# Kernel tuning notes

Hardware: AMD Instinct MI355X
Metric: run time of the kernel (lower is better)

The kernel has to match this reference:

```python
import jax, jax.numpy as jnp
import numpy as np

B, N, G, T = 512, 10000, 2048, 131072  # batch, gene sets, agg groups, total flat indices

def setup_inputs() -> dict:
    key = jax.random.key(0)
    k1, k2, k3 = jax.random.split(key, 3)
    gene_set_features = jax.random.normal(k1, (B, N), dtype=jnp.float32)
    flat_indices = jax.random.randint(k2, (T,), 0, N)          # which gene-set column each slot reads
    segment_ids = jnp.sort(jax.random.randint(k3, (T,), 0, G))  # which agg group each slot belongs to
    return {"gene_set_features": gene_set_features,
            "flat_indices": flat_indices,
            "segment_ids": segment_ids,
            "num_groups": G}

def reference(gene_set_features, flat_indices, segment_ids, num_groups):
    # Ragged per-group mean pooling (pooling_type='mean'), CSR-style in one pass.
    gathered = gene_set_features[:, flat_indices]            # [B, T]
    sums = jax.ops.segment_sum(gathered.T, segment_ids,
                               num_segments=num_groups)      # [G, B]
    counts = jax.ops.segment_sum(jnp.ones((flat_indices.shape[0],),
                                          dtype=gene_set_features.dtype),
                                 segment_ids, num_segments=num_groups)  # [G]
    means = sums / jnp.maximum(counts, 1.0)[:, None]         # empty groups -> 0, matching zeros init
    return means.T                                           # [B, G]
```

## Files before the change

### kernel.cpp

```cpp
#include <hip/hip_runtime.h>


__device__ __forceinline__ unsigned bf16rne(float f) {
    unsigned u = __float_as_uint(f);
    return (u + 0x7fffu + ((u >> 16) & 1u)) >> 16;
}

__global__ __launch_bounds__(256) void pa_prep(const float* __restrict__ feat,
                                               const int* __restrict__ seg,
                                               unsigned short* __restrict__ featT,
                                               int* __restrict__ offs,
                                               int N, int T, int G, int nXBlocks) {
    if (blockIdx.y == 8) {
        int stride = nXBlocks * 256;
        for (int t = blockIdx.x * 256 + threadIdx.x; t < T; t += stride) {
            int cur  = seg[t];
            int prev = (t == 0) ? -1 : seg[t - 1];
            for (int g = prev + 1; g <= cur; ++g) offs[g] = t;
            if (t == T - 1) {
                for (int g = cur + 1; g <= G; ++g) offs[g] = T;
            }
        }
        return;
    }

    __shared__ float tile[64][65];
    const int n0 = blockIdx.x * 64;
    const int b0 = blockIdx.y * 64;
    const int tid = threadIdx.x;
    const int r  = tid >> 4;
    const int c4 = tid & 15;

    if (n0 + 64 <= N) {
        #pragma unroll
        for (int i = 0; i < 4; ++i) {
            int b = r + 16 * i;
            const float4 v = *(const float4*)&feat[(size_t)(b0 + b) * N + n0 + c4 * 4];
            tile[b][c4 * 4 + 0] = v.x;
            tile[b][c4 * 4 + 1] = v.y;
            tile[b][c4 * 4 + 2] = v.z;
            tile[b][c4 * 4 + 3] = v.w;
        }
    } else {
        #pragma unroll
        for (int i = 0; i < 4; ++i) {
            int b = r + 16 * i;
            #pragma unroll
            for (int j = 0; j < 4; ++j) {
                int n = n0 + c4 * 4 + j;
                tile[b][c4 * 4 + j] = (n < N) ? feat[(size_t)(b0 + b) * N + n] : 0.0f;
            }
        }
    }
    __syncthreads();

    uint2* outu = (uint2*)featT;
    #pragma unroll
    for (int i = 0; i < 4; ++i) {
        int nl = r + 16 * i;
        int n = n0 + nl;
        if (n >= N) continue;
        uint2 u;
        u.x = bf16rne(tile[c4 * 4 + 0][nl]) | (bf16rne(tile[c4 * 4 + 1][nl]) << 16);
        u.y = bf16rne(tile[c4 * 4 + 2][nl]) | (bf16rne(tile[c4 * 4 + 3][nl]) << 16);
        outu[(size_t)n * 128 + (b0 >> 2) + c4] = u;
    }
}

#define ACC8(v)                                   \
    do {                                          \
        a0 += __uint_as_float((v).x << 16);       \
        a1 += __uint_as_float((v).x);             \
        a2 += __uint_as_float((v).y << 16);       \
        a3 += __uint_as_float((v).y);             \
        a4 += __uint_as_float((v).z << 16);       \
        a5 += __uint_as_float((v).z);             \
        a6 += __uint_as_float((v).w << 16);       \
        a7 += __uint_as_float((v).w);             \
    } while (0)

__global__ __launch_bounds__(256) void pa_gather_mean_bf16(
    const unsigned short* __restrict__ featT,
    const int* __restrict__ idxs,
    const int* __restrict__ offs,
    float* __restrict__ out,
    int G) {
    const int chunk = blockIdx.x & 7;
    const int wave  = threadIdx.x >> 6;
    const int g     = (blockIdx.x >> 3) * 4 + wave;
    const int lane  = threadIdx.x & 63;
    const int lane_b = lane & 7;
    const int slot   = lane >> 3;

    const int s = offs[g];
    const int e = offs[g + 1];
    const int cnt = e - s;

    const char* __restrict__ fbase = (const char*)featT + chunk * 128 + lane_b * 16;

    float a0 = 0.f, a1 = 0.f, a2 = 0.f, a3 = 0.f,
          a4 = 0.f, a5 = 0.f, a6 = 0.f, a7 = 0.f;

    int w = s;
    int nrem = cnt;
    int myidx = (s + lane < e) ? idxs[s + lane] : 0;

    while (nrem >= 64) {
        int cur = myidx;
        w += 64;
        nrem -= 64;
        if (nrem > 0) myidx = (w + lane < e) ? idxs[w + lane] : 0;
        #pragma unroll
        for (int k = 0; k < 8; ++k) {
            int ridx = __shfl(cur, slot + 8 * k);
            uint4 v = *(const uint4*)(fbase + ((size_t)(unsigned)(ridx << 10)));
            ACC8(v);
        }
    }
    if (nrem > 0) {
        int cur = myidx;
        #pragma unroll
        for (int k = 0; k < 8; ++k) {
            int li = slot + 8 * k;
            int ridx = __shfl(cur, li);
            if (li < nrem) {
                uint4 v = *(const uint4*)(fbase + ((size_t)(unsigned)(ridx << 10)));
                ACC8(v);
            }
        }
    }

    a0 += __shfl_xor(a0, 8); a0 += __shfl_xor(a0, 16); a0 += __shfl_xor(a0, 32);
    a1 += __shfl_xor(a1, 8); a1 += __shfl_xor(a1, 16); a1 += __shfl_xor(a1, 32);
    a2 += __shfl_xor(a2, 8); a2 += __shfl_xor(a2, 16); a2 += __shfl_xor(a2, 32);
    a3 += __shfl_xor(a3, 8); a3 += __shfl_xor(a3, 16); a3 += __shfl_xor(a3, 32);
    a4 += __shfl_xor(a4, 8); a4 += __shfl_xor(a4, 16); a4 += __shfl_xor(a4, 32);
    a5 += __shfl_xor(a5, 8); a5 += __shfl_xor(a5, 16); a5 += __shfl_xor(a5, 32);
    a6 += __shfl_xor(a6, 8); a6 += __shfl_xor(a6, 16); a6 += __shfl_xor(a6, 32);
    a7 += __shfl_xor(a7, 8); a7 += __shfl_xor(a7, 16); a7 += __shfl_xor(a7, 32);

    __shared__ float tile[4][64];
    if (slot == 0) {
        float inv = 1.0f / (float)(cnt > 0 ? cnt : 1);
        int bl = lane_b * 8;
        tile[wave][bl + 0] = a0 * inv;
        tile[wave][bl + 1] = a1 * inv;
        tile[wave][bl + 2] = a2 * inv;
        tile[wave][bl + 3] = a3 * inv;
        tile[wave][bl + 4] = a4 * inv;
        tile[wave][bl + 5] = a5 * inv;
        tile[wave][bl + 6] = a6 * inv;
        tile[wave][bl + 7] = a7 * inv;
    }
    __syncthreads();

    int b_local = threadIdx.x >> 2;
    int gi      = threadIdx.x & 3;
    int gg      = (blockIdx.x >> 3) * 4 + gi;
    out[(size_t)(chunk * 64 + b_local) * G + gg] = tile[gi][b_local];
}

__global__ __launch_bounds__(256) void pa_group_mean_direct(
    const float* __restrict__ feat, const int* __restrict__ flat_indices,
    const int* __restrict__ segment_ids, float* __restrict__ out,
    int T, int B, int N, int G) {
    const int g = blockIdx.x;
    const int tid = threadIdx.x;
    __shared__ int sb[2];
    __shared__ int s_idx[256];
    if (tid < 2) {
        int target = g + tid;
        int lo = 0, hi = T;
        while (lo < hi) {
            int mid = (lo + hi) >> 1;
            if (segment_ids[mid] < target) lo = mid + 1; else hi = mid;
        }
        sb[tid] = lo;
    }
    __syncthreads();
    const int s = sb[0], e = sb[1];
    const int cnt = e - s;
    int b0 = tid * 2, b1 = tid * 2 + 1;
    float x0 = 0.f, x1 = 0.f;
    for (int base = s; base < e; base += 256) {
        int k = base + tid;
        if (k < e) s_idx[tid] = flat_indices[k];
        __syncthreads();
        int m = min(256, e - base);
        for (int jj = 0; jj < m; ++jj) {
            int idx = s_idx[jj];
            if (b0 < B) x0 += feat[(long)b0 * N + idx];
            if (b1 < B) x1 += feat[(long)b1 * N + idx];
        }
        __syncthreads();
    }
    float inv = 1.0f / (float)(cnt > 0 ? cnt : 1);
    if (b0 < B) out[(long)b0 * G + g] = x0 * inv;
    if (b1 < B) out[(long)b1 * G + g] = x1 * inv;
}

extern "C" void kernel_launch(void* const* d_in, const int* in_sizes, int n_in,
                              void* d_out, int out_size, void* d_ws, size_t ws_size,
                              hipStream_t stream) {
    const float* feat          = (const float*)d_in[0];
    const int*   flat_indices  = (const int*)d_in[1];
    const int*   segment_ids   = (const int*)d_in[2];
    float*       out           = (float*)d_out;

    const int B = 512;
    const int N = in_sizes[0] / B;
    const int T = in_sizes[1];
    const int G = out_size / B;

    size_t featT_bytes = (size_t)N * B * sizeof(unsigned short);
    size_t need = featT_bytes + (size_t)(G + 1) * sizeof(int);
    if (ws_size >= need && B == 512 && (G % 4) == 0 && T >= 1) {
        unsigned short* featT = (unsigned short*)d_ws;
        int* offs = (int*)((char*)d_ws + featT_bytes);

        int nXBlocks = (N + 63) / 64;
        dim3 g1(nXBlocks, 9);
        pa_prep<<<g1, 256, 0, stream>>>(feat, segment_ids, featT, offs, N, T, G, nXBlocks);

        pa_gather_mean_bf16<<<(G / 4) * 8, 256, 0, stream>>>(featT, flat_indices, offs,
                                                             out, G);
    } else {
        pa_group_mean_direct<<<G, 256, 0, stream>>>(feat, flat_indices, segment_ids,
                                                    out, T, B, N, G);
    }
}
```

Measured before the change: 26.51 us.

## Process two groups per wave in gather and flatten prep grid ordering

The gather kernel now gives each wave two segment groups with separate accumulator sets, interleaving their 64-index windows so more independent loads are in flight. It launches half as many blocks and writes output as float2. The prep kernel switches to a 1D grid where the 8 batch chunks for one N tile are adjacent, and the offset-building blocks sit at the end. This trades more registers and some load imbalance between paired groups for more memory-level parallelism per wave.

```diff
diff --git a/kernel.cpp b/kernel.cpp
--- a/kernel.cpp
+++ b/kernel.cpp
@@ -10,10 +10,13 @@
                                                const int* __restrict__ seg,
                                                unsigned short* __restrict__ featT,
                                                int* __restrict__ offs,
-                                               int N, int T, int G, int nXBlocks) {
-    if (blockIdx.y == 8) {
-        int stride = nXBlocks * 256;
-        for (int t = blockIdx.x * 256 + threadIdx.x; t < T; t += stride) {
+                                               int N, int T, int G, int nTiles) {
+    const int x = blockIdx.x;
+    const int nTr = nTiles * 8;
+    if (x >= nTr) {
+        int s = x - nTr;
+        if (s >= 157) return;
+        for (int t = s * 256 + threadIdx.x; t < T; t += 157 * 256) {
             int cur  = seg[t];
             int prev = (t == 0) ? -1 : seg[t - 1];
             for (int g = prev + 1; g <= cur; ++g) offs[g] = t;
@@ -25,8 +28,9 @@
     }
 
     __shared__ float tile[64][65];
-    const int n0 = blockIdx.x * 64;
-    const int b0 = blockIdx.y * 64;
+    const int c  = x & 7;
+    const int n0 = (x >> 3) * 64;
+    const int b0 = c * 64;
     const int tid = threadIdx.x;
     const int r  = tid >> 4;
     const int c4 = tid & 15;
@@ -67,7 +71,7 @@
     }
 }
 
-#define ACC8(v)                                   \
+#define ACC8(v, a0, a1, a2, a3, a4, a5, a6, a7)   \
     do {                                          \
         a0 += __uint_as_float((v).x << 16);       \
         a1 += __uint_as_float((v).x);             \
@@ -79,6 +83,32 @@
         a7 += __uint_as_float((v).w);             \
     } while (0)
 
+#define FULLWIN(cur, a0, a1, a2, a3, a4, a5, a6, a7)                         \
+    do {                                                                     \
+        _Pragma("unroll")                                                    \
+        for (int k = 0; k < 8; ++k) {                                        \
+            int ridx = __shfl((cur), slot + 8 * k);                          \
+            uint4 v = *(const uint4*)(fbase + ((size_t)(unsigned)(ridx << 10))); \
+            ACC8(v, a0, a1, a2, a3, a4, a5, a6, a7);                         \
+        }                                                                    \
+    } while (0)
+
+#define TAILWIN(cur, nr, a0, a1, a2, a3, a4, a5, a6, a7)                     \
+    do {                                                                     \
+        _Pragma("unroll")                                                    \
+        for (int k = 0; k < 8; ++k) {                                        \
+            int li = slot + 8 * k;                                           \
+            int ridx = __shfl((cur), li);                                    \
+            if (li < (nr)) {                                                 \
+                uint4 v = *(const uint4*)(fbase + ((size_t)(unsigned)(ridx << 10))); \
+                ACC8(v, a0, a1, a2, a3, a4, a5, a6, a7);                     \
+            }                                                                \
+        }                                                                    \
+    } while (0)
+
+#define RED8(a) \
+    a += __shfl_xor(a, 8); a += __shfl_xor(a, 16); a += __shfl_xor(a, 32)
+
 __global__ __launch_bounds__(256) void pa_gather_mean_bf16(
     const unsigned short* __restrict__ featT,
     const int* __restrict__ idxs,
@@ -86,78 +116,88 @@
     float* __restrict__ out,
     int G) {
     const int chunk = blockIdx.x & 7;
+    const int i     = blockIdx.x >> 3;
     const int wave  = threadIdx.x >> 6;
-    const int g     = (blockIdx.x >> 3) * 4 + wave;
     const int lane  = threadIdx.x & 63;
     const int lane_b = lane & 7;
     const int slot   = lane >> 3;
 
-    const int s = offs[g];
-    const int e = offs[g + 1];
-    const int cnt = e - s;
+    const int g0 = i * 8 + wave * 2;
+    const int g1 = g0 + 1;
+    const int s0 = offs[g0], e0 = offs[g0 + 1];
+    const int s1 = offs[g1], e1 = offs[g1 + 1];
+    const int cnt0 = e0 - s0, cnt1 = e1 - s1;
 
     const char* __restrict__ fbase = (const char*)featT + chunk * 128 + lane_b * 16;
 
     float a0 = 0.f, a1 = 0.f, a2 = 0.f, a3 = 0.f,
           a4 = 0.f, a5 = 0.f, a6 = 0.f, a7 = 0.f;
-
-    int w = s;
-    int nrem = cnt;
-    int myidx = (s + lane < e) ? idxs[s + lane] : 0;
-
-    while (nrem >= 64) {
-        int cur = myidx;
-        w += 64;
-        nrem -= 64;
-        if (nrem > 0) myidx = (w + lane < e) ? idxs[w + lane] : 0;
-        #pragma unroll
-        for (int k = 0; k < 8; ++k) {
-            int ridx = __shfl(cur, slot + 8 * k);
-            uint4 v = *(const uint4*)(fbase + ((size_t)(unsigned)(ridx << 10)));
-            ACC8(v);
-        }
-    }
-    if (nrem > 0) {
-        int cur = myidx;
-        #pragma unroll
-        for (int k = 0; k < 8; ++k) {
-            int li = slot + 8 * k;
-            int ridx = __shfl(cur, li);
-            if (li < nrem) {
-                uint4 v = *(const uint4*)(fbase + ((size_t)(unsigned)(ridx << 10)));
-                ACC8(v);
-            }
-        }
-    }
-
-    a0 += __shfl_xor(a0, 8); a0 += __shfl_xor(a0, 16); a0 += __shfl_xor(a0, 32);
-    a1 += __shfl_xor(a1, 8); a1 += __shfl_xor(a1, 16); a1 += __shfl_xor(a1, 32);
-    a2 += __shfl_xor(a2, 8); a2 += __shfl_xor(a2, 16); a2 += __shfl_xor(a2, 32);
-    a3 += __shfl_xor(a3, 8); a3 += __shfl_xor(a3, 16); a3 += __shfl_xor(a3, 32);
-    a4 += __shfl_xor(a4, 8); a4 += __shfl_xor(a4, 16); a4 += __shfl_xor(a4, 32);
-    a5 += __shfl_xor(a5, 8); a5 += __shfl_xor(a5, 16); a5 += __shfl_xor(a5, 32);
-    a6 += __shfl_xor(a6, 8); a6 += __shfl_xor(a6, 16); a6 += __shfl_xor(a6, 32);
-    a7 += __shfl_xor(a7, 8); a7 += __shfl_xor(a7, 16); a7 += __shfl_xor(a7, 32);
-
-    __shared__ float tile[4][64];
+    float b0 = 0.f, b1 = 0.f, b2 = 0.f, b3 = 0.f,
+          b4 = 0.f, b5 = 0.f, b6 = 0.f, b7 = 0.f;
+
+    int w0 = s0, n0 = cnt0;
+    int w1 = s1, n1 = cnt1;
+    int id0 = (w0 + lane < e0) ? idxs[w0 + lane] : 0;
+    int id1 = (w1 + lane < e1) ? idxs[w1 + lane] : 0;
+
+    while (n0 >= 64 && n1 >= 64) {
+        int c0 = id0, c1 = id1;
+        w0 += 64; n0 -= 64;
+        w1 += 64; n1 -= 64;
+        if (n0 > 0) id0 = (w0 + lane < e0) ? idxs[w0 + lane] : 0;
+        if (n1 > 0) id1 = (w1 + lane < e1) ? idxs[w1 + lane] : 0;
+        FULLWIN(c0, a0, a1, a2, a3, a4, a5, a6, a7);
+        FULLWIN(c1, b0, b1, b2, b3, b4, b5, b6, b7);
+    }
+    while (n0 >= 64) {
+        int c0 = id0;
+        w0 += 64; n0 -= 64;
+        if (n0 > 0) id0 = (w0 + lane < e0) ? idxs[w0 + lane] : 0;
+        FULLWIN(c0, a0, a1, a2, a3, a4, a5, a6, a7);
+    }
+    while (n1 >= 64) {
+        int c1 = id1;
+        w1 += 64; n1 -= 64;
+        if (n1 > 0) id1 = (w1 + lane < e1) ? idxs[w1 + lane] : 0;
+        FULLWIN(c1, b0, b1, b2, b3, b4, b5, b6, b7);
+    }
+    if (n0 > 0) TAILWIN(id0, n0, a0, a1, a2, a3, a4, a5, a6, a7);
+    if (n1 > 0) TAILWIN(id1, n1, b0, b1, b2, b3, b4, b5, b6, b7);
+
+    RED8(a0); RED8(a1); RED8(a2); RED8(a3); RED8(a4); RED8(a5); RED8(a6); RED8(a7);
+    RED8(b0); RED8(b1); RED8(b2); RED8(b3); RED8(b4); RED8(b5); RED8(b6); RED8(b7);
+
+    __shared__ float gtile[8][64];
     if (slot == 0) {
-        float inv = 1.0f / (float)(cnt > 0 ? cnt : 1);
         int bl = lane_b * 8;
-        tile[wave][bl + 0] = a0 * inv;
-        tile[wave][bl + 1] = a1 * inv;
-        tile[wave][bl + 2] = a2 * inv;
-        tile[wave][bl + 3] = a3 * inv;
-        tile[wave][bl + 4] = a4 * inv;
-        tile[wave][bl + 5] = a5 * inv;
-        tile[wave][bl + 6] = a6 * inv;
-        tile[wave][bl + 7] = a7 * inv;
+        float inv0 = 1.0f / (float)(cnt0 > 0 ? cnt0 : 1);
+        float inv1 = 1.0f / (float)(cnt1 > 0 ? cnt1 : 1);
+        int r0 = wave * 2, r1 = wave * 2 + 1;
+        gtile[r0][bl + 0] = a0 * inv0;
+        gtile[r0][bl + 1] = a1 * inv0;
+        gtile[r0][bl + 2] = a2 * inv0;
+        gtile[r0][bl + 3] = a3 * inv0;
+        gtile[r0][bl + 4] = a4 * inv0;
+        gtile[r0][bl + 5] = a5 * inv0;
+        gtile[r0][bl + 6] = a6 * inv0;
+        gtile[r0][bl + 7] = a7 * inv0;
+        gtile[r1][bl + 0] = b0 * inv1;
+        gtile[r1][bl + 1] = b1 * inv1;
+        gtile[r1][bl + 2] = b2 * inv1;
+        gtile[r1][bl + 3] = b3 * inv1;
+        gtile[r1][bl + 4] = b4 * inv1;
+        gtile[r1][bl + 5] = b5 * inv1;
+        gtile[r1][bl + 6] = b6 * inv1;
+        gtile[r1][bl + 7] = b7 * inv1;
     }
     __syncthreads();
 
-    int b_local = threadIdx.x >> 2;
-    int gi      = threadIdx.x & 3;
-    int gg      = (blockIdx.x >> 3) * 4 + gi;
-    out[(size_t)(chunk * 64 + b_local) * G + gg] = tile[gi][b_local];
+    int bb = threadIdx.x >> 2;
+    int gp = threadIdx.x & 3;
+    float2 r2;
+    r2.x = gtile[gp * 2 + 0][bb];
+    r2.y = gtile[gp * 2 + 1][bb];
+    *(float2*)&out[(size_t)(chunk * 64 + bb) * G + i * 8 + gp * 2] = r2;
 }
 
 __global__ __launch_bounds__(256) void pa_group_mean_direct(
@@ -180,7 +220,7 @@
     __syncthreads();
     const int s = sb[0], e = sb[1];
     const int cnt = e - s;
-    int b0 = tid * 2, b1 = tid * 2 + 1;
+    int p0 = tid * 2, p1 = tid * 2 + 1;
     float x0 = 0.f, x1 = 0.f;
     for (int base = s; base < e; base += 256) {
         int k = base + tid;
@@ -189,14 +229,14 @@
         int m = min(256, e - base);
         for (int jj = 0; jj < m; ++jj) {
             int idx = s_idx[jj];
-            if (b0 < B) x0 += feat[(long)b0 * N + idx];
-            if (b1 < B) x1 += feat[(long)b1 * N + idx];
+            if (p0 < B) x0 += feat[(long)p0 * N + idx];
+            if (p1 < B) x1 += feat[(long)p1 * N + idx];
         }
         __syncthreads();
     }
     float inv = 1.0f / (float)(cnt > 0 ? cnt : 1);
-    if (b0 < B) out[(long)b0 * G + g] = x0 * inv;
-    if (b1 < B) out[(long)b1 * G + g] = x1 * inv;
+    if (p0 < B) out[(long)p0 * G + g] = x0 * inv;
+    if (p1 < B) out[(long)p1 * G + g] = x1 * inv;
 }
 
 extern "C" void kernel_launch(void* const* d_in, const int* in_sizes, int n_in,
@@ -214,15 +254,17 @@
 
     size_t featT_bytes = (size_t)N * B * sizeof(unsigned short);
     size_t need = featT_bytes + (size_t)(G + 1) * sizeof(int);
-    if (ws_size >= need && B == 512 && (G % 4) == 0 && T >= 1) {
+    if (ws_size >= need && B == 512 && (G % 8) == 0 && T >= 1) {
         unsigned short* featT = (unsigned short*)d_ws;
         int* offs = (int*)((char*)d_ws + featT_bytes);
 
-        int nXBlocks = (N + 63) / 64;
-        dim3 g1(nXBlocks, 9);
-        pa_prep<<<g1, 256, 0, stream>>>(feat, segment_ids, featT, offs, N, T, G, nXBlocks);
-
-        pa_gather_mean_bf16<<<(G / 4) * 8, 256, 0, stream>>>(featT, flat_indices, offs,
+        int nTiles = (N + 63) / 64;
+        int nBlocks = nTiles * 8 + 157;
+        nBlocks = (nBlocks + 7) & ~7;
+        pa_prep<<<nBlocks, 256, 0, stream>>>(feat, segment_ids, featT, offs,
+                                             N, T, G, nTiles);
+
+        pa_gather_mean_bf16<<<(G / 8) * 8, 256, 0, stream>>>(featT, flat_indices, offs,
                                                              out, G);
     } else {
         pa_group_mean_direct<<<G, 256, 0, stream>>>(feat, flat_indices, segment_ids,
```

New measurement: 27.16 us. +2.4%, slower.

## Persistent-grid prep with folded offsets pass; two groups per wave in gather

Applied to the files above, without the earlier changes.

The transpose/bf16 prep kernel now runs on a fixed 1024-block grid that loops over tiles. The last 157 blocks additionally build the segment offsets, replacing the separate ninth grid row. The gather kernel now has each wave process two groups sequentially, halving the block count, and writes the output as float2 pairs for wider stores. The aim is to cut launch/tail imbalance in prep and per-block overhead in gather, at the cost of less parallelism per group and some load imbalance on the offset-building blocks.

```diff
diff --git a/kernel.cpp b/kernel.cpp
--- a/kernel.cpp
+++ b/kernel.cpp
@@ -10,10 +10,62 @@
                                                const int* __restrict__ seg,
                                                unsigned short* __restrict__ featT,
                                                int* __restrict__ offs,
-                                               int N, int T, int G, int nXBlocks) {
-    if (blockIdx.y == 8) {
-        int stride = nXBlocks * 256;
-        for (int t = blockIdx.x * 256 + threadIdx.x; t < T; t += stride) {
+                                               int N, int T, int G, int nTiles) {
+    const int x = blockIdx.x;
+    const int nTr = nTiles * 8;
+    const int tid = threadIdx.x;
+
+    __shared__ float tile[64][65];
+    const int r  = tid >> 4;
+    const int c4 = tid & 15;
+
+    for (int tau = x; tau < nTr; tau += 1024) {
+        const int c  = tau & 7;
+        const int n0 = (tau >> 3) * 64;
+        const int b0 = c * 64;
+
+        if (n0 + 64 <= N) {
+            #pragma unroll
+            for (int i = 0; i < 4; ++i) {
+                int b = r + 16 * i;
+                const float4 v = *(const float4*)&feat[(size_t)(b0 + b) * N + n0 + c4 * 4];
+                tile[b][c4 * 4 + 0] = v.x;
+                tile[b][c4 * 4 + 1] = v.y;
+                tile[b][c4 * 4 + 2] = v.z;
+                tile[b][c4 * 4 + 3] = v.w;
+            }
+        } else {
+            #pragma unroll
+            for (int i = 0; i < 4; ++i) {
+                int b = r + 16 * i;
+                #pragma unroll
+                for (int j = 0; j < 4; ++j) {
+                    int n = n0 + c4 * 4 + j;
+                    tile[b][c4 * 4 + j] = (n < N) ? feat[(size_t)(b0 + b) * N + n] : 0.0f;
+                }
+            }
+        }
+        __syncthreads();
+
+        uint2* outu = (uint2*)featT;
+        #pragma unroll
+        for (int i = 0; i < 4; ++i) {
+            int nl = r + 16 * i;
+            int n = n0 + nl;
+            if (n < N) {
+                uint2 u;
+                u.x = bf16rne(tile[c4 * 4 + 0][nl]) | (bf16rne(tile[c4 * 4 + 1][nl]) << 16);
+                u.y = bf16rne(tile[c4 * 4 + 2][nl]) | (bf16rne(tile[c4 * 4 + 3][nl]) << 16);
+                outu[(size_t)n * 128 + (b0 >> 2) + c4] = u;
+            }
+        }
+        __syncthreads();
+    }
+
+    const int sBase = 1024 - 157;
+    if (x >= sBase) {
+        int s = x - sBase;
+        for (int t = s * 256 + tid; t < T; t += 157 * 256) {
             int cur  = seg[t];
             int prev = (t == 0) ? -1 : seg[t - 1];
             for (int g = prev + 1; g <= cur; ++g) offs[g] = t;
@@ -21,63 +73,19 @@
                 for (int g = cur + 1; g <= G; ++g) offs[g] = T;
             }
         }
-        return;
-    }
-
-    __shared__ float tile[64][65];
-    const int n0 = blockIdx.x * 64;
-    const int b0 = blockIdx.y * 64;
-    const int tid = threadIdx.x;
-    const int r  = tid >> 4;
-    const int c4 = tid & 15;
-
-    if (n0 + 64 <= N) {
-        #pragma unroll
-        for (int i = 0; i < 4; ++i) {
-            int b = r + 16 * i;
-            const float4 v = *(const float4*)&feat[(size_t)(b0 + b) * N + n0 + c4 * 4];
-            tile[b][c4 * 4 + 0] = v.x;
-            tile[b][c4 * 4 + 1] = v.y;
-            tile[b][c4 * 4 + 2] = v.z;
-            tile[b][c4 * 4 + 3] = v.w;
-        }
-    } else {
-        #pragma unroll
-        for (int i = 0; i < 4; ++i) {
-            int b = r + 16 * i;
-            #pragma unroll
-            for (int j = 0; j < 4; ++j) {
-                int n = n0 + c4 * 4 + j;
-                tile[b][c4 * 4 + j] = (n < N) ? feat[(size_t)(b0 + b) * N + n] : 0.0f;
-            }
-        }
-    }
-    __syncthreads();
-
-    uint2* outu = (uint2*)featT;
-    #pragma unroll
-    for (int i = 0; i < 4; ++i) {
-        int nl = r + 16 * i;
-        int n = n0 + nl;
-        if (n >= N) continue;
-        uint2 u;
-        u.x = bf16rne(tile[c4 * 4 + 0][nl]) | (bf16rne(tile[c4 * 4 + 1][nl]) << 16);
-        u.y = bf16rne(tile[c4 * 4 + 2][nl]) | (bf16rne(tile[c4 * 4 + 3][nl]) << 16);
-        outu[(size_t)n * 128 + (b0 >> 2) + c4] = u;
-    }
-}
-
-#define ACC8(v)                                   \
-    do {                                          \
-        a0 += __uint_as_float((v).x << 16);       \
-        a1 += __uint_as_float((v).x);             \
-        a2 += __uint_as_float((v).y << 16);       \
-        a3 += __uint_as_float((v).y);             \
-        a4 += __uint_as_float((v).z << 16);       \
-        a5 += __uint_as_float((v).z);             \
-        a6 += __uint_as_float((v).w << 16);       \
-        a7 += __uint_as_float((v).w);             \
+    }
+}
+
+#define ACC8(v)                                                          \
+    do {                                                                 \
+        A0.x += __uint_as_float((v).x << 16); A0.y += __uint_as_float((v).x); \
+        A1.x += __uint_as_float((v).y << 16); A1.y += __uint_as_float((v).y); \
+        A2.x += __uint_as_float((v).z << 16); A2.y += __uint_as_float((v).z); \
+        A3.x += __uint_as_float((v).w << 16); A3.y += __uint_as_float((v).w); \
     } while (0)
+
+#define RED8(a) \
+    a += __shfl_xor(a, 8); a += __shfl_xor(a, 16); a += __shfl_xor(a, 32)
 
 __global__ __launch_bounds__(256) void pa_gather_mean_bf16(
     const unsigned short* __restrict__ featT,
@@ -86,78 +94,80 @@
     float* __restrict__ out,
     int G) {
     const int chunk = blockIdx.x & 7;
+    const int i     = blockIdx.x >> 3;
     const int wave  = threadIdx.x >> 6;
-    const int g     = (blockIdx.x >> 3) * 4 + wave;
     const int lane  = threadIdx.x & 63;
     const int lane_b = lane & 7;
     const int slot   = lane >> 3;
 
-    const int s = offs[g];
-    const int e = offs[g + 1];
-    const int cnt = e - s;
-
     const char* __restrict__ fbase = (const char*)featT + chunk * 128 + lane_b * 16;
 
-    float a0 = 0.f, a1 = 0.f, a2 = 0.f, a3 = 0.f,
-          a4 = 0.f, a5 = 0.f, a6 = 0.f, a7 = 0.f;
-
-    int w = s;
-    int nrem = cnt;
-    int myidx = (s + lane < e) ? idxs[s + lane] : 0;
-
-    while (nrem >= 64) {
-        int cur = myidx;
-        w += 64;
-        nrem -= 64;
-        if (nrem > 0) myidx = (w + lane < e) ? idxs[w + lane] : 0;
-        #pragma unroll
-        for (int k = 0; k < 8; ++k) {
-            int ridx = __shfl(cur, slot + 8 * k);
-            uint4 v = *(const uint4*)(fbase + ((size_t)(unsigned)(ridx << 10)));
-            ACC8(v);
-        }
-    }
-    if (nrem > 0) {
-        int cur = myidx;
-        #pragma unroll
-        for (int k = 0; k < 8; ++k) {
-            int li = slot + 8 * k;
-            int ridx = __shfl(cur, li);
-            if (li < nrem) {
+    __shared__ float gtile[8][64];
+
+    #pragma unroll
+    for (int q = 0; q < 2; ++q) {
+        const int g = i * 8 + wave * 2 + q;
+        const int s = offs[g];
+        const int e = offs[g + 1];
+        const int cnt = e - s;
+
+        float2 A0 = make_float2(0.f, 0.f), A1 = make_float2(0.f, 0.f),
+               A2 = make_float2(0.f, 0.f), A3 = make_float2(0.f, 0.f);
+
+        int w = s;
+        int nrem = cnt;
+        int myidx = (s + lane < e) ? idxs[s + lane] : 0;
+
+        while (nrem >= 64) {
+            int cur = myidx;
+            w += 64;
+            nrem -= 64;
+            if (nrem > 0) myidx = (w + lane < e) ? idxs[w + lane] : 0;
+            #pragma unroll
+            for (int k = 0; k < 8; ++k) {
+                int ridx = __shfl(cur, slot + 8 * k);
                 uint4 v = *(const uint4*)(fbase + ((size_t)(unsigned)(ridx << 10)));
                 ACC8(v);
             }
         }
-    }
-
-    a0 += __shfl_xor(a0, 8); a0 += __shfl_xor(a0, 16); a0 += __shfl_xor(a0, 32);
-    a1 += __shfl_xor(a1, 8); a1 += __shfl_xor(a1, 16); a1 += __shfl_xor(a1, 32);
-    a2 += __shfl_xor(a2, 8); a2 += __shfl_xor(a2, 16); a2 += __shfl_xor(a2, 32);
-    a3 += __shfl_xor(a3, 8); a3 += __shfl_xor(a3, 16); a3 += __shfl_xor(a3, 32);
-    a4 += __shfl_xor(a4, 8); a4 += __shfl_xor(a4, 16); a4 += __shfl_xor(a4, 32);
-    a5 += __shfl_xor(a5, 8); a5 += __shfl_xor(a5, 16); a5 += __shfl_xor(a5, 32);
-    a6 += __shfl_xor(a6, 8); a6 += __shfl_xor(a6, 16); a6 += __shfl_xor(a6, 32);
-    a7 += __shfl_xor(a7, 8); a7 += __shfl_xor(a7, 16); a7 += __shfl_xor(a7, 32);
-
-    __shared__ float tile[4][64];
-    if (slot == 0) {
-        float inv = 1.0f / (float)(cnt > 0 ? cnt : 1);
-        int bl = lane_b * 8;
-        tile[wave][bl + 0] = a0 * inv;
-        tile[wave][bl + 1] = a1 * inv;
-        tile[wave][bl + 2] = a2 * inv;
-        tile[wave][bl + 3] = a3 * inv;
-        tile[wave][bl + 4] = a4 * inv;
-        tile[wave][bl + 5] = a5 * inv;
-        tile[wave][bl + 6] = a6 * inv;
-        tile[wave][bl + 7] = a7 * inv;
+        if (nrem > 0) {
+            int cur = myidx;
+            #pragma unroll
+            for (int k = 0; k < 8; ++k) {
+                int li = slot + 8 * k;
+                int ridx = __shfl(cur, li);
+                if (li < nrem) {
+                    uint4 v = *(const uint4*)(fbase + ((size_t)(unsigned)(ridx << 10)));
+                    ACC8(v);
+                }
+            }
+        }
+
+        RED8(A0.x); RED8(A0.y); RED8(A1.x); RED8(A1.y);
+        RED8(A2.x); RED8(A2.y); RED8(A3.x); RED8(A3.y);
+
+        if (slot == 0) {
+            float inv = 1.0f / (float)(cnt > 0 ? cnt : 1);
+            int rrow = wave * 2 + q;
+            int bl = lane_b * 8;
+            gtile[rrow][bl + 0] = A0.x * inv;
+            gtile[rrow][bl + 1] = A0.y * inv;
+            gtile[rrow][bl + 2] = A1.x * inv;
+            gtile[rrow][bl + 3] = A1.y * inv;
+            gtile[rrow][bl + 4] = A2.x * inv;
+            gtile[rrow][bl + 5] = A2.y * inv;
+            gtile[rrow][bl + 6] = A3.x * inv;
+            gtile[rrow][bl + 7] = A3.y * inv;
+        }
     }
     __syncthreads();
 
-    int b_local = threadIdx.x >> 2;
-    int gi      = threadIdx.x & 3;
-    int gg      = (blockIdx.x >> 3) * 4 + gi;
-    out[(size_t)(chunk * 64 + b_local) * G + gg] = tile[gi][b_local];
+    int bb = threadIdx.x >> 2;
+    int gp = threadIdx.x & 3;
+    float2 r2;
+    r2.x = gtile[gp * 2 + 0][bb];
+    r2.y = gtile[gp * 2 + 1][bb];
+    *(float2*)&out[(size_t)(chunk * 64 + bb) * G + i * 8 + gp * 2] = r2;
 }
 
 __global__ __launch_bounds__(256) void pa_group_mean_direct(
@@ -180,7 +190,7 @@
     __syncthreads();
     const int s = sb[0], e = sb[1];
     const int cnt = e - s;
-    int b0 = tid * 2, b1 = tid * 2 + 1;
+    int p0 = tid * 2, p1 = tid * 2 + 1;
     float x0 = 0.f, x1 = 0.f;
     for (int base = s; base < e; base += 256) {
         int k = base + tid;
@@ -189,14 +199,14 @@
         int m = min(256, e - base);
         for (int jj = 0; jj < m; ++jj) {
             int idx = s_idx[jj];
-            if (b0 < B) x0 += feat[(long)b0 * N + idx];
-            if (b1 < B) x1 += feat[(long)b1 * N + idx];
+            if (p0 < B) x0 += feat[(long)p0 * N + idx];
+            if (p1 < B) x1 += feat[(long)p1 * N + idx];
         }
         __syncthreads();
     }
     float inv = 1.0f / (float)(cnt > 0 ? cnt : 1);
-    if (b0 < B) out[(long)b0 * G + g] = x0 * inv;
-    if (b1 < B) out[(long)b1 * G + g] = x1 * inv;
+    if (p0 < B) out[(long)p0 * G + g] = x0 * inv;
+    if (p1 < B) out[(long)p1 * G + g] = x1 * inv;
 }
 
 extern "C" void kernel_launch(void* const* d_in, const int* in_sizes, int n_in,
@@ -214,15 +224,16 @@
 
     size_t featT_bytes = (size_t)N * B * sizeof(unsigned short);
     size_t need = featT_bytes + (size_t)(G + 1) * sizeof(int);
-    if (ws_size >= need && B == 512 && (G % 4) == 0 && T >= 1) {
+    int nTiles = (N + 63) / 64;
+    if (ws_size >= need && B == 512 && (G % 8) == 0 && T >= 1 &&
+        nTiles * 8 <= 2048 && nTiles >= 157) {
         unsigned short* featT = (unsigned short*)d_ws;
         int* offs = (int*)((char*)d_ws + featT_bytes);
 
-        int nXBlocks = (N + 63) / 64;
-        dim3 g1(nXBlocks, 9);
-        pa_prep<<<g1, 256, 0, stream>>>(feat, segment_ids, featT, offs, N, T, G, nXBlocks);
-
-        pa_gather_mean_bf16<<<(G / 4) * 8, 256, 0, stream>>>(featT, flat_indices, offs,
+        pa_prep<<<1024, 256, 0, stream>>>(feat, segment_ids, featT, offs,
+                                          N, T, G, nTiles);
+
+        pa_gather_mean_bf16<<<(G / 8) * 8, 256, 0, stream>>>(featT, flat_indices, offs,
                                                              out, G);
     } else {
         pa_group_mean_direct<<<G, 256, 0, stream>>>(feat, flat_indices, segment_ids,
```

New measurement: 25.83 us. 1.03x faster.
